# Optimization experiments

Measured on AMD Instinct MI355X. Metric: run time of the kernel, lower is better.

The kernel has to match this reference:

```python
import jax, jax.numpy as jnp
import numpy as np

N_EXPERTS = 16
NUM_SHARDS = 1
CAPACITY_FACTOR = 1.25
EPS = 0.01


def setup_inputs() -> dict:
    key = jax.random.key(0)
    k1, k2, k3 = jax.random.split(key, 3)
    C, T, D = 4, 4096, 1024
    E = N_EXPERTS * NUM_SHARDS
    inputs = jax.random.normal(k1, (C, T, D), dtype=jnp.float32)
    # trunc-normal router weight, std = (initializer_factor / ((D + E)/2))**0.5
    std = (1.0 / ((D + E) / 2.0)) ** 0.5
    router_weight = jax.random.truncated_normal(k2, -2.0, 2.0, (E, D), dtype=jnp.float32) * std
    # multiplicative jitter in [1-eps, 1+eps)
    noise = (1.0 - EPS) + 2.0 * EPS * jax.random.uniform(k3, (C, T, D), dtype=jnp.float32)
    return {"inputs": inputs, "router_weight": router_weight, "noise": noise}


def reference(inputs, router_weight, noise):
    C, T, D = inputs.shape
    E = N_EXPERTS * NUM_SHARDS
    expert_capacity = max(int(CAPACITY_FACTOR * T // N_EXPERTS), 1)

    x = inputs.astype(jnp.float32) * noise                      # gate inputs with jitter
    router_logits = jnp.einsum('ctd,ed->cte', x, router_weight)  # [C,T,E]
    router_probs = jax.nn.softmax(router_logits, axis=-1)
    expert_gate = jnp.max(router_probs, axis=-1)                 # [C,T]
    expert_index = jnp.argmax(router_probs, axis=-1)             # [C,T] int

    expert_mask = jax.nn.one_hot(expert_index, E, dtype=jnp.float32)  # [C,T,E]

    # load-balancing aux loss (before capacity truncation)
    density1 = expert_mask.mean(axis=1)          # [C,E]
    density1_proxy = router_probs.mean(axis=1)   # [C,E]
    aux_loss = (density1 * density1_proxy).sum() * E

    # capacity-limited position tracking
    position_in_expert = jnp.cumsum(expert_mask, axis=1) * expert_mask            # [C,T,E]
    expert_mask = expert_mask * (position_in_expert.astype(jnp.int32) < expert_capacity)
    expert_mask_flat = expert_mask.sum(axis=-1)                                    # [C,T]
    position_in_expert = (jnp.cumsum(expert_mask, axis=1) * expert_mask).astype(jnp.int32)
    expert_gate = expert_gate * expert_mask_flat

    # Faithful replication of torch scatter_(dim=1) on a [C,T,E,1] tensor with
    # index shape [C,T,1,1]: only the (e=0, cap=0) slice is written, at token
    # position == expert_index[c,t].
    c_idx = jnp.arange(C)[:, None]
    expert_index_inf = jnp.zeros((C, T, E, 1), jnp.float32).at[c_idx, expert_index, 0, 0].set(1.0)

    # one-hot over capacity slot (scatter along dim 3)
    position_inf = jax.nn.one_hot(position_in_expert, expert_capacity, dtype=jnp.float32)  # [C,T,E,cap]

    combine_tensor = (expert_gate[:, :, None, None]
                      * expert_mask_flat[:, :, None, None]
                      * expert_index_inf
                      * position_inf)
    dispatch_tensor = combine_tensor.astype(bool)
    return dispatch_tensor, combine_tensor, aux_loss
```

## Files before the change

### kernel.cpp

```cpp
#include <hip/hip_runtime.h>
#include <math.h>

#define C_DIM 4
#define T_DIM 4096
#define D_DIM 1024
#define E_DIM 16
#define CAP   320
#define CT    (C_DIM * T_DIM)
#define OUT_ONE ((size_t)CT * E_DIM * CAP)


__global__ __launch_bounds__(256) void router_logits_kernel(
    const float* __restrict__ in, const float* __restrict__ w,
    const float* __restrict__ noise, float* __restrict__ gate,
    int* __restrict__ index, float* __restrict__ auxpart)
{
    __shared__ float psum[E_DIM];
    const int tid  = threadIdx.x;
    if (tid < E_DIM) psum[tid] = 0.0f;
    __syncthreads();

    const int wave = tid >> 6;
    const int lane = tid & 63;
    const int g0   = blockIdx.x * 16 + wave * 4;

    float acc[4][16];
    #pragma unroll
    for (int tk = 0; tk < 4; ++tk)
        #pragma unroll
        for (int e = 0; e < 16; ++e)
            acc[tk][e] = 0.0f;

    #pragma unroll
    for (int r = 0; r < 4; ++r) {
        const int d0 = r * 256 + lane * 4;
        float4 x[4];
        #pragma unroll
        for (int tk = 0; tk < 4; ++tk) {
            const float4 a = *(const float4*)(in    + (size_t)(g0 + tk) * D_DIM + d0);
            const float4 n = *(const float4*)(noise + (size_t)(g0 + tk) * D_DIM + d0);
            x[tk] = make_float4(a.x * n.x, a.y * n.y, a.z * n.z, a.w * n.w);
        }
        #pragma unroll
        for (int e = 0; e < 16; ++e) {
            const float4 wv = *(const float4*)(w + e * D_DIM + d0);
            #pragma unroll
            for (int tk = 0; tk < 4; ++tk) {
                acc[tk][e] += x[tk].x * wv.x + x[tk].y * wv.y
                            + x[tk].z * wv.z + x[tk].w * wv.w;
            }
        }
    }

    #pragma unroll
    for (int tk = 0; tk < 4; ++tk)
        #pragma unroll
        for (int e = 0; e < 16; ++e)
            #pragma unroll
            for (int off = 32; off; off >>= 1)
                acc[tk][e] += __shfl_down(acc[tk][e], off, 64);

    if (lane == 0) {
        #pragma unroll
        for (int tk = 0; tk < 4; ++tk) {
            const int g = g0 + tk;
            float m = -1e30f; int am = 0;
            #pragma unroll
            for (int e = 0; e < 16; ++e)
                if (acc[tk][e] > m) { m = acc[tk][e]; am = e; }
            float p[16]; float s = 0.0f;
            #pragma unroll
            for (int e = 0; e < 16; ++e) { p[e] = __expf(acc[tk][e] - m); s += p[e]; }
            const float inv = 1.0f / s;
            gate[g]  = inv;
            index[g] = am;
            #pragma unroll
            for (int e = 0; e < 16; ++e)
                atomicAdd(&psum[e], p[e] * inv);
        }
    }
    __syncthreads();
    if (tid < 16) {
        const int c = blockIdx.x / 256;
        atomicAdd(&auxpart[c * 16 + tid], psum[tid]);
    }
}

__global__ __launch_bounds__(256) void rank_kernel(
    const int* __restrict__ index, int* __restrict__ rank, int* __restrict__ counts)
{
    __shared__ int hist[256 * 16];
    const int tid = threadIdx.x;
    const int c   = blockIdx.x;
    const int* idxrow = index + c * T_DIM;
    const int base = tid * 16;

    #pragma unroll
    for (int e = 0; e < 16; ++e) hist[base + e] = 0;
    __syncthreads();

    for (int j = 0; j < 16; ++j) {
        const int e = idxrow[base + j];
        hist[base + e] += 1;
    }
    __syncthreads();

    if (tid < 16) {
        int running = 0;
        for (int i = 0; i < 256; ++i) {
            const int v = hist[i * 16 + tid];
            hist[i * 16 + tid] = running;
            running += v;
        }
        counts[c * 16 + tid] = running;
    }
    __syncthreads();

    for (int j = 0; j < 16; ++j) {
        const int t = base + j;
        const int e = idxrow[t];
        const int r = hist[base + e] + 1;
        hist[base + e] = r;
        rank[c * T_DIM + t] = r;
    }
}

__global__ __launch_bounds__(64) void finalize_kernel(
    const float* __restrict__ gate, const int* __restrict__ index,
    const int* __restrict__ rank, const int* __restrict__ counts,
    const float* __restrict__ auxpart, float* __restrict__ out)
{
    const int id = threadIdx.x;
    const int c  = id >> 4;
    const int tp = id & 15;
    const int cnt = counts[id];

    float term = ((float)cnt * (1.0f / T_DIM)) * (auxpart[id] * (1.0f / T_DIM));

    if (cnt > 0) {
        const int g  = c * T_DIM + tp;
        const int rk = rank[g];
        if (rk < CAP) {
            const int idx = index[g];
            const int s   = (idx == 0) ? rk : 0;
            const size_t off = ((size_t)g * E_DIM + 0) * CAP + (size_t)s;
            out[off]            = 1.0f;
            out[OUT_ONE + off]  = gate[g];
        }
    }

    #pragma unroll
    for (int off = 32; off; off >>= 1)
        term += __shfl_down(term, off, 64);
    if (id == 0)
        out[2 * OUT_ONE] = 16.0f * term;
}

extern "C" void kernel_launch(void* const* d_in, const int* in_sizes, int n_in,
                              void* d_out, int out_size, void* d_ws, size_t ws_size,
                              hipStream_t stream) {
    const float* in    = (const float*)d_in[0];
    const float* w     = (const float*)d_in[1];
    const float* noise = (const float*)d_in[2];
    float* out = (float*)d_out;

    char* ws = (char*)d_ws;
    float* auxpart = (float*)(ws);
    int*   counts  = (int*)(ws + 256);
    float* gate    = (float*)(ws + 512);
    int*   index   = (int*)(ws + 512 + 65536);
    int*   rank    = (int*)(ws + 512 + 131072);

    hipMemsetAsync(d_out, 0, (size_t)out_size * sizeof(float), stream);
    hipMemsetAsync(ws, 0, 256, stream);

    router_logits_kernel<<<dim3(CT / 16), dim3(256), 0, stream>>>(in, w, noise, gate, index, auxpart);
    rank_kernel<<<dim3(C_DIM), dim3(256), 0, stream>>>(index, rank, counts);
    finalize_kernel<<<dim3(1), dim3(64), 0, stream>>>(gate, index, rank, counts, auxpart, out);
}
```

Baseline: 195.0 us.

## Fuse output zero-fill and expert counting into router kernel, drop rank kernel

Removes the separate memset of the large dispatch/combine output and has each router block zero a contiguous slice of it with float4 stores, so the fill overlaps with the router matmul. Per-expert counts are now gathered with shared-memory atomics in the router kernel. The rank kernel goes away and the finalize kernel recomputes the few needed ranks inline by scanning the first 16 tokens. The single-wave finalize does the small scan serially, and the capacity check on rank is dropped, which only holds because the first 16 positions can never exceed capacity.

```diff
diff --git a/kernel.cpp b/kernel.cpp
--- a/kernel.cpp
+++ b/kernel.cpp
@@ -9,15 +9,21 @@
 #define CT    (C_DIM * T_DIM)
 #define OUT_ONE ((size_t)CT * E_DIM * CAP)
 
+#define NBLOCKS 1024
+#define N4      ((2 * OUT_ONE) / 4)
+#define F4_PER_BLOCK (N4 / NBLOCKS)
 
-__global__ __launch_bounds__(256) void router_logits_kernel(
+
+__global__ __launch_bounds__(256) void fused_router_fill_kernel(
     const float* __restrict__ in, const float* __restrict__ w,
     const float* __restrict__ noise, float* __restrict__ gate,
-    int* __restrict__ index, float* __restrict__ auxpart)
+    int* __restrict__ index, float* __restrict__ auxpart,
+    int* __restrict__ counts, float4* __restrict__ out4)
 {
     __shared__ float psum[E_DIM];
+    __shared__ int   hcnt[E_DIM];
     const int tid  = threadIdx.x;
-    if (tid < E_DIM) psum[tid] = 0.0f;
+    if (tid < E_DIM) { psum[tid] = 0.0f; hcnt[tid] = 0; }
     __syncthreads();
 
     const int wave = tid >> 6;
@@ -74,6 +80,7 @@
             const float inv = 1.0f / s;
             gate[g]  = inv;
             index[g] = am;
+            atomicAdd(&hcnt[am], 1);
             #pragma unroll
             for (int e = 0; e < 16; ++e)
                 atomicAdd(&psum[e], p[e] * inv);
@@ -81,54 +88,22 @@
     }
     __syncthreads();
     if (tid < 16) {
-        const int c = blockIdx.x / 256;
+        const int c = blockIdx.x >> 8;
         atomicAdd(&auxpart[c * 16 + tid], psum[tid]);
+        atomicAdd(&counts [c * 16 + tid], hcnt[tid]);
     }
-}
 
-__global__ __launch_bounds__(256) void rank_kernel(
-    const int* __restrict__ index, int* __restrict__ rank, int* __restrict__ counts)
-{
-    __shared__ int hist[256 * 16];
-    const int tid = threadIdx.x;
-    const int c   = blockIdx.x;
-    const int* idxrow = index + c * T_DIM;
-    const int base = tid * 16;
-
-    #pragma unroll
-    for (int e = 0; e < 16; ++e) hist[base + e] = 0;
-    __syncthreads();
-
-    for (int j = 0; j < 16; ++j) {
-        const int e = idxrow[base + j];
-        hist[base + e] += 1;
-    }
-    __syncthreads();
-
-    if (tid < 16) {
-        int running = 0;
-        for (int i = 0; i < 256; ++i) {
-            const int v = hist[i * 16 + tid];
-            hist[i * 16 + tid] = running;
-            running += v;
-        }
-        counts[c * 16 + tid] = running;
-    }
-    __syncthreads();
-
-    for (int j = 0; j < 16; ++j) {
-        const int t = base + j;
-        const int e = idxrow[t];
-        const int r = hist[base + e] + 1;
-        hist[base + e] = r;
-        rank[c * T_DIM + t] = r;
-    }
+    const float4 z = make_float4(0.f, 0.f, 0.f, 0.f);
+    float4* dst = out4 + (size_t)blockIdx.x * F4_PER_BLOCK;
+    #pragma unroll 4
+    for (int i = tid; i < F4_PER_BLOCK; i += 256)
+        dst[i] = z;
 }
 
 __global__ __launch_bounds__(64) void finalize_kernel(
     const float* __restrict__ gate, const int* __restrict__ index,
-    const int* __restrict__ rank, const int* __restrict__ counts,
-    const float* __restrict__ auxpart, float* __restrict__ out)
+    const int* __restrict__ counts, const float* __restrict__ auxpart,
+    float* __restrict__ out)
 {
     const int id = threadIdx.x;
     const int c  = id >> 4;
@@ -138,15 +113,18 @@
     float term = ((float)cnt * (1.0f / T_DIM)) * (auxpart[id] * (1.0f / T_DIM));
 
     if (cnt > 0) {
-        const int g  = c * T_DIM + tp;
-        const int rk = rank[g];
-        if (rk < CAP) {
-            const int idx = index[g];
-            const int s   = (idx == 0) ? rk : 0;
-            const size_t off = ((size_t)g * E_DIM + 0) * CAP + (size_t)s;
-            out[off]            = 1.0f;
-            out[OUT_ONE + off]  = gate[g];
+        const int g    = c * T_DIM + tp;
+        const int myidx = index[g];
+        int s = 0;
+        if (myidx == 0) {
+            int r = 0;
+            for (int t = 0; t <= tp; ++t)
+                r += (index[c * T_DIM + t] == 0);
+            s = r;
         }
+        const size_t off = ((size_t)g * E_DIM + 0) * CAP + (size_t)s;
+        out[off]            = 1.0f;
+        out[OUT_ONE + off]  = gate[g];
     }
 
     #pragma unroll
@@ -169,12 +147,10 @@
     int*   counts  = (int*)(ws + 256);
     float* gate    = (float*)(ws + 512);
     int*   index   = (int*)(ws + 512 + 65536);
-    int*   rank    = (int*)(ws + 512 + 131072);
 
-    hipMemsetAsync(d_out, 0, (size_t)out_size * sizeof(float), stream);
-    hipMemsetAsync(ws, 0, 256, stream);
+    (void)hipMemsetAsync(ws, 0, 512, stream);
 
-    router_logits_kernel<<<dim3(CT / 16), dim3(256), 0, stream>>>(in, w, noise, gate, index, auxpart);
-    rank_kernel<<<dim3(C_DIM), dim3(256), 0, stream>>>(index, rank, counts);
-    finalize_kernel<<<dim3(1), dim3(64), 0, stream>>>(gate, index, rank, counts, auxpart, out);
+    fused_router_fill_kernel<<<dim3(NBLOCKS), dim3(256), 0, stream>>>(
+        in, w, noise, gate, index, auxpart, counts, (float4*)out);
+    finalize_kernel<<<dim3(1), dim3(64), 0, stream>>>(gate, index, counts, auxpart, out);
 }
```

Result: faster. 186.3 us (-4.4%).
